# Kernel tuning notes

Measured on AMD Instinct MI355X. Metric: run time of the kernel, lower is better.

## Reference

```python
import jax, jax.numpy as jnp
import numpy as np

E = 1024   # embedding_dim
H = 16     # num_head
D = 64     # dim_head (E == H*D)
R = 8      # LoRA rank
BATCH = 2
SEQ = 2048
EPS = 1e-6


def setup_inputs() -> dict:
    key = jax.random.key(0)
    ks = jax.random.split(key, 16)
    s = 0.02
    return {
        "y": jax.random.normal(ks[0], (BATCH, SEQ, E), jnp.float32),
        "Wqkv": jax.random.normal(ks[1], (3 * E, E), jnp.float32) * s,
        "bqkv": jax.random.normal(ks[2], (3 * E,), jnp.float32) * s,
        "Wmsa": jax.random.normal(ks[3], (E, E), jnp.float32) * s,
        "Bq": jax.random.normal(ks[4], (E, R), jnp.float32) * s,
        "Aq": jax.random.normal(ks[5], (R, E), jnp.float32) * s,
        "Bk": jax.random.normal(ks[6], (E, R), jnp.float32) * s,
        "Ak": jax.random.normal(ks[7], (R, E), jnp.float32) * s,
        "Bv": jax.random.normal(ks[8], (E, R), jnp.float32) * s,
        "Av": jax.random.normal(ks[9], (R, E), jnp.float32) * s,
        "Bo": jax.random.normal(ks[10], (E, R), jnp.float32) * s,
        "Ao": jax.random.normal(ks[11], (R, E), jnp.float32) * s,
        "gamma": jnp.ones((E,), jnp.float32),
        "beta": jnp.zeros((E,), jnp.float32),
        "i": 0,
    }


def reference(y, Wqkv, bqkv, Wmsa, Bq, Aq, Bk, Ak, Bv, Av, Bo, Ao, gamma, beta, i):
    B, S, En = y.shape
    # fused QKV projection: nn.Linear -> y @ W.T + b
    qkv = (y @ Wqkv.T + bqkv).reshape(B, S, 3, H, D).transpose(2, 0, 3, 1, 4)
    Q, K, V = qkv[0], qkv[1], qkv[2]          # each [B,H,S,D]

    def lora_delta(Bw, Aw):
        # torch: y @ (B.weight @ A.weight), reshaped to heads
        return (y @ (Bw @ Aw)).reshape(B, S, H, D).transpose(0, 2, 1, 3)

    Q = Q + lora_delta(Bq, Aq)
    K = K + lora_delta(Bk, Ak)
    V = V + lora_delta(Bv, Av)

    scale = jnp.asarray(np.sqrt(D), y.dtype)
    scores = jnp.einsum('bhqd,bhkd->bhqk', Q, K) / scale
    attn = jax.nn.softmax(scores, axis=-1)
    o = jnp.einsum('bhqk,bhkd->bhqd', attn, V)          # [B,H,S,D]
    o = o.transpose(0, 2, 1, 3).reshape(B, S, H * D)    # [B,S,E]

    msa = o @ Wmsa.T + o @ (Bo @ Ao)
    res = msa + y

    mu = jnp.mean(res, axis=-1, keepdims=True)
    var = jnp.var(res, axis=-1, keepdims=True)
    return (res - mu) * jax.lax.rsqrt(var + EPS) * gamma + beta
```

## Files before the change

kernel.cpp:

```cpp
#include <hip/hip_runtime.h>
#include <hip/hip_bf16.h>
#include <stdint.h>

typedef __attribute__((ext_vector_type(8))) short short8;
typedef __attribute__((ext_vector_type(4))) float f32x4;

typedef const __attribute__((address_space(1))) void gv_t;
typedef __attribute__((address_space(3))) void lv_t;

#define SCQ 0.18033688011112042f

__device__ __forceinline__ void gl_lds16(const void* g, void* l) {
    __builtin_amdgcn_global_load_lds((gv_t*)g, (lv_t*)l, 16, 0, 0);
}

__device__ __forceinline__ unsigned short f2bf(float f) {
    union { float f; unsigned int u; } v; v.f = f;
    unsigned int r = v.u + 0x7fffu + ((v.u >> 16) & 1u);
    return (unsigned short)(r >> 16);
}

__device__ __forceinline__ unsigned int pack2bf(float a, float b) {
    union { __hip_bfloat162 h2; unsigned int u; } cv;
    cv.h2 = __float22bfloat162_rn(make_float2(a, b));
    return cv.u;
}

__device__ __forceinline__ f32x4 zero4() { f32x4 z = {0.f, 0.f, 0.f, 0.f}; return z; }

__global__ void k_prep(const float* __restrict__ y,
                       const float* __restrict__ Wqkv, const float* __restrict__ Wmsa,
                       const float* __restrict__ Bq, const float* __restrict__ Aq,
                       const float* __restrict__ Bk, const float* __restrict__ Ak,
                       const float* __restrict__ Bv, const float* __restrict__ Av,
                       const float* __restrict__ Bo, const float* __restrict__ Ao,
                       unsigned short* __restrict__ wout, unsigned short* __restrict__ yb) {
    const int bid = blockIdx.x;
    if (bid < 16384) {
        int idx = bid * 256 + threadIdx.x;
        int n = idx >> 10, k = idx & 1023;
        int sel = n >> 10, n0 = n & 1023;
        const float* Bp = (sel == 0) ? Bq : (sel == 1) ? Bk : (sel == 2) ? Bv : Bo;
        const float* Ap = (sel == 0) ? Aq : (sel == 1) ? Ak : (sel == 2) ? Av : Ao;
        float acc = (sel < 3) ? Wqkv[idx] : Wmsa[idx - 3145728];
        #pragma unroll
        for (int r = 0; r < 8; ++r) acc += Bp[k * 8 + r] * Ap[r * 1024 + n0];
        wout[idx] = f2bf(acc * ((sel == 0) ? SCQ : 1.0f));
    } else {
        int i = ((bid - 16384) * 256 + threadIdx.x) * 4;
        float4 v = *(const float4*)(y + i);
        union { unsigned short u[4]; uint2 w; } o;
        o.u[0] = f2bf(v.x); o.u[1] = f2bf(v.y); o.u[2] = f2bf(v.z); o.u[3] = f2bf(v.w);
        *(uint2*)(yb + i) = o.w;
    }
}

template <int TM, int EPI, int MINW>
__global__ __launch_bounds__(256, MINW) void k_gemm(const unsigned short* __restrict__ Ag,
                                                    const unsigned short* __restrict__ Bg,
                                                    const float* __restrict__ bias,
                                                    const float* __restrict__ yres,
                                                    unsigned short* __restrict__ vtg,
                                                    void* __restrict__ Cout,
                                                    int M, int N, int K) {
    constexpr int WAVES_N = 256 / TM;
    constexpr int WN = TM / 2;
    constexpr int NI = WN / 16;
    constexpr int ACALLS = TM / 64;
    __shared__ unsigned short As[2][TM * 32];
    __shared__ unsigned short Bs[2][128 * 32];
    const int flat = threadIdx.x;
    const int m0 = blockIdx.y * TM, n0 = blockIdx.x * 128;
    const int lane = flat & 63, wave = flat >> 6;
    const int l16 = lane & 15, quad = lane >> 4;
    const int wm = (wave / WAVES_N) * 64, wn = (wave % WAVES_N) * WN;

    f32x4 acc[4][NI];
    #pragma unroll
    for (int mi = 0; mi < 4; ++mi)
        #pragma unroll
        for (int ni = 0; ni < NI; ++ni) acc[mi][ni] = zero4();

    const unsigned short* ap = Ag + (size_t)(m0 + (flat >> 2)) * K + (flat & 3) * 8;
    const unsigned short* bp = Bg + (size_t)(n0 + (flat >> 2)) * K + (flat & 3) * 8;
    const size_t rstep = (size_t)64 * K;

    #pragma unroll
    for (int c = 0; c < ACALLS; ++c) gl_lds16(ap + c * rstep, &As[0][c * 2048 + flat * 8]);
    gl_lds16(bp,         &Bs[0][flat * 8]);
    gl_lds16(bp + rstep, &Bs[0][2048 + flat * 8]);
    ap += 32; bp += 32;
    __syncthreads();

    for (int k0 = 0; k0 < K; k0 += 32) {
        const int cur = (k0 >> 5) & 1;
        if (k0 + 32 < K) {
            const int nxt = cur ^ 1;
            #pragma unroll
            for (int c = 0; c < ACALLS; ++c) gl_lds16(ap + c * rstep, &As[nxt][c * 2048 + flat * 8]);
            gl_lds16(bp,         &Bs[nxt][flat * 8]);
            gl_lds16(bp + rstep, &Bs[nxt][2048 + flat * 8]);
            ap += 32; bp += 32;
        }

        short8 af[4], bfr[NI];
        #pragma unroll
        for (int i = 0; i < 4; ++i) af[i] = *(const short8*)&As[cur][(wm + i * 16 + l16) * 32 + quad * 8];
        #pragma unroll
        for (int i = 0; i < NI; ++i) bfr[i] = *(const short8*)&Bs[cur][(wn + i * 16 + l16) * 32 + quad * 8];
        #pragma unroll
        for (int mi = 0; mi < 4; ++mi)
            #pragma unroll
            for (int ni = 0; ni < NI; ++ni)
                acc[mi][ni] = __builtin_amdgcn_mfma_f32_16x16x32_bf16(af[mi], bfr[ni], acc[mi][ni], 0, 0, 0);

        __syncthreads();
    }

    if (EPI == 0) {
        unsigned short* C = (unsigned short*)Cout;
        if (n0 < 2048) {
            #pragma unroll
            for (int ni = 0; ni < NI; ++ni) {
                int col = n0 + wn + ni * 16 + l16;
                float bv = bias[col] * ((col < 1024) ? SCQ : 1.0f);
                #pragma unroll
                for (int mi = 0; mi < 4; ++mi) {
                    int row = m0 + wm + mi * 16 + quad * 4;
                    #pragma unroll
                    for (int r = 0; r < 4; ++r)
                        C[(size_t)(row + r) * N + col] = f2bf(acc[mi][ni][r] + bv);
                }
            }
        } else {
            #pragma unroll
            for (int ni = 0; ni < NI; ++ni) {
                int col = n0 + wn + ni * 16 + l16;
                float bv = bias[col];
                int hh = (col - 2048) >> 6, dd = col & 63;
                unsigned short* vrow0 = vtg + (size_t)(hh * 64 + dd) * 2048;
                #pragma unroll
                for (int mi = 0; mi < 4; ++mi) {
                    int row = m0 + wm + mi * 16 + quad * 4;
                    int bb = row >> 11, ss = row & 2047;
                    uint2 w;
                    w.x = pack2bf(acc[mi][ni][0] + bv, acc[mi][ni][1] + bv);
                    w.y = pack2bf(acc[mi][ni][2] + bv, acc[mi][ni][3] + bv);
                    *(uint2*)(vrow0 + (size_t)bb * 2097152 + ss) = w;
                }
            }
        }
    } else {
        float* C = (float*)Cout;
        #pragma unroll
        for (int ni = 0; ni < NI; ++ni) {
            int col = n0 + wn + ni * 16 + l16;
            #pragma unroll
            for (int mi = 0; mi < 4; ++mi) {
                int row = m0 + wm + mi * 16 + quad * 4;
                #pragma unroll
                for (int r = 0; r < 4; ++r)
                    C[(size_t)(row + r) * N + col] = acc[mi][ni][r] + yres[(size_t)(row + r) * N + col];
            }
        }
    }
}

__global__ __launch_bounds__(256, 3) void k_attn(const unsigned short* __restrict__ qkv,
                                                 const unsigned short* __restrict__ vtg,
                                                 unsigned short* __restrict__ o) {
    __shared__ unsigned short LDS[24576];
    unsigned short* Qs = LDS;
    unsigned short* Ps = LDS;
    unsigned short* Ks0 = LDS + 8192;
    unsigned short* Vt0 = LDS + 16384;

    const int t = threadIdx.x;
    const int lane = t & 63, wave = t >> 6;
    const int l16 = lane & 15, quad = lane >> 4;
    const int l8 = l16 & 7;
    const int q0 = blockIdx.x * 128;
    const int h = blockIdx.y, b = blockIdx.z;

    const unsigned short* qbase = qkv + (size_t)(b * 2048) * 3072 + h * 64;
    const unsigned short* kbase = qbase + 1024;
    const unsigned short* vtbase = vtg + (size_t)((b * 16 + h) * 64) * 2048;

    #pragma unroll
    for (int i = 0; i < 4; ++i) {
        int B = i * 256 + t;
        int row = B >> 3, c = (B & 7) ^ (row & 7);
        gl_lds16(qbase + (size_t)(q0 + row) * 3072 + c * 8, &Qs[B * 8]);
    }

    const int B0 = t, B1 = t + 256;
    const int r0 = B0 >> 3, c0 = (B0 & 7) ^ (r0 & 7);
    const int r1 = B1 >> 3, c1 = (B1 & 7) ^ (r1 & 7);
    const unsigned short* kp0 = kbase + (size_t)r0 * 3072 + c0 * 8;
    const unsigned short* kp1 = kbase + (size_t)r1 * 3072 + c1 * 8;
    const unsigned short* vp0 = vtbase + (size_t)r0 * 2048 + c0 * 8;
    const unsigned short* vp1 = vtbase + (size_t)r1 * 2048 + c1 * 8;

    gl_lds16(kp0, &Ks0[B0 * 8]);
    gl_lds16(kp1, &Ks0[B1 * 8]);
    gl_lds16(vp0, &Vt0[B0 * 8]);
    gl_lds16(vp1, &Vt0[B1 * 8]);
    kp0 += 64 * 3072; kp1 += 64 * 3072; vp0 += 64; vp1 += 64;

    __syncthreads();

    short8 qf[2][2];
    #pragma unroll
    for (int ni = 0; ni < 2; ++ni)
        #pragma unroll
        for (int kk = 0; kk < 2; ++kk)
            qf[ni][kk] = *(const short8*)&Qs[(wave * 32 + ni * 16 + l16) * 64 + ((kk * 4 + quad) ^ l8) * 8];

    __syncthreads();

    f32x4 acc_o[2][4];
    #pragma unroll
    for (int mo = 0; mo < 2; ++mo)
        #pragma unroll
        for (int nd = 0; nd < 4; ++nd) acc_o[mo][nd] = zero4();
    f32x4 acc_l[2] = {zero4(), zero4()};
    short8 ones;
    #pragma unroll
    for (int i = 0; i < 8; ++i) ones[i] = (short)0x3F80;

    for (int j = 0; j < 32; ++j) {
        const unsigned short* Ks = Ks0 + (j & 1) * 4096;
        const unsigned short* Vt = Vt0 + (j & 1) * 4096;

        if (j < 31) {
            unsigned short* Kn = Ks0 + ((j + 1) & 1) * 4096;
            unsigned short* Vn = Vt0 + ((j + 1) & 1) * 4096;
            gl_lds16(kp0, &Kn[B0 * 8]);
            gl_lds16(kp1, &Kn[B1 * 8]);
            gl_lds16(vp0, &Vn[B0 * 8]);
            gl_lds16(vp1, &Vn[B1 * 8]);
            kp0 += 64 * 3072; kp1 += 64 * 3072; vp0 += 64; vp1 += 64;
        }

        f32x4 sacc[4][2];
        #pragma unroll
        for (int mi = 0; mi < 4; ++mi)
            #pragma unroll
            for (int ni = 0; ni < 2; ++ni) sacc[mi][ni] = zero4();
        #pragma unroll
        for (int kk = 0; kk < 2; ++kk)
            #pragma unroll
            for (int mi = 0; mi < 4; ++mi) {
                short8 kf = *(const short8*)&Ks[(mi * 16 + l16) * 64 + ((kk * 4 + quad) ^ l8) * 8];
                #pragma unroll
                for (int ni = 0; ni < 2; ++ni)
                    sacc[mi][ni] = __builtin_amdgcn_mfma_f32_16x16x32_bf16(kf, qf[ni][kk], sacc[mi][ni], 0, 0, 0);
            }

        #pragma unroll
        for (int ni = 0; ni < 2; ++ni) {
            int qrow = wave * 32 + ni * 16 + l16;
            #pragma unroll
            for (int mi = 0; mi < 4; ++mi) {
                float p0 = __builtin_amdgcn_exp2f(sacc[mi][ni][0]);
                float p1 = __builtin_amdgcn_exp2f(sacc[mi][ni][1]);
                float p2 = __builtin_amdgcn_exp2f(sacc[mi][ni][2]);
                float p3 = __builtin_amdgcn_exp2f(sacc[mi][ni][3]);
                uint2 w; w.x = pack2bf(p0, p1); w.y = pack2bf(p2, p3);
                *(uint2*)&Ps[qrow * 64 + ((2 * mi + (quad >> 1)) ^ l8) * 8 + (quad & 1) * 4] = w;
            }
        }

        #pragma unroll
        for (int kk = 0; kk < 2; ++kk) {
            short8 pf[2];
            #pragma unroll
            for (int mo = 0; mo < 2; ++mo) {
                pf[mo] = *(const short8*)&Ps[(wave * 32 + mo * 16 + l16) * 64 + ((kk * 4 + quad) ^ l8) * 8];
                acc_l[mo] = __builtin_amdgcn_mfma_f32_16x16x32_bf16(pf[mo], ones, acc_l[mo], 0, 0, 0);
            }
            #pragma unroll
            for (int nd = 0; nd < 4; ++nd) {
                short8 vf = *(const short8*)&Vt[(nd * 16 + l16) * 64 + ((kk * 4 + quad) ^ l8) * 8];
                #pragma unroll
                for (int mo = 0; mo < 2; ++mo)
                    acc_o[mo][nd] = __builtin_amdgcn_mfma_f32_16x16x32_bf16(pf[mo], vf, acc_o[mo][nd], 0, 0, 0);
            }
        }

        __syncthreads();
    }

    #pragma unroll
    for (int mo = 0; mo < 2; ++mo)
        #pragma unroll
        for (int rr = 0; rr < 4; ++rr) {
            float inv = 1.0f / acc_l[mo][rr];
            int qg = q0 + wave * 32 + mo * 16 + quad * 4 + rr;
            size_t base = ((size_t)(b * 2048 + qg)) * 1024 + h * 64;
            #pragma unroll
            for (int nd = 0; nd < 4; ++nd)
                o[base + nd * 16 + l16] = f2bf(acc_o[mo][nd][rr] * inv);
        }
}

__global__ __launch_bounds__(256) void k_ln(const float* __restrict__ res,
                                            const float* __restrict__ g,
                                            const float* __restrict__ be,
                                            float* __restrict__ out) {
    __shared__ float red[8];
    const int row = blockIdx.x, t = threadIdx.x;
    const float* x = res + (size_t)row * 1024;
    float4 v = *(const float4*)(x + t * 4);
    float s = v.x + v.y + v.z + v.w;
    float sq = v.x * v.x + v.y * v.y + v.z * v.z + v.w * v.w;
    #pragma unroll
    for (int off = 32; off; off >>= 1) { s += __shfl_down(s, off); sq += __shfl_down(sq, off); }
    if ((t & 63) == 0) { red[t >> 6] = s; red[4 + (t >> 6)] = sq; }
    __syncthreads();
    float ts = red[0] + red[1] + red[2] + red[3];
    float tq = red[4] + red[5] + red[6] + red[7];
    float mu = ts * (1.f / 1024.f);
    float var = tq * (1.f / 1024.f) - mu * mu;
    float rstd = rsqrtf(var + 1e-6f);
    float4 gg = *(const float4*)(g + t * 4);
    float4 bb = *(const float4*)(be + t * 4);
    float4 ov;
    ov.x = (v.x - mu) * rstd * gg.x + bb.x;
    ov.y = (v.y - mu) * rstd * gg.y + bb.y;
    ov.z = (v.z - mu) * rstd * gg.z + bb.z;
    ov.w = (v.w - mu) * rstd * gg.w + bb.w;
    *(float4*)(out + (size_t)row * 1024 + t * 4) = ov;
}

extern "C" void kernel_launch(void* const* d_in, const int* in_sizes, int n_in,
                              void* d_out, int out_size, void* d_ws, size_t ws_size,
                              hipStream_t stream) {
    (void)in_sizes; (void)n_in; (void)out_size; (void)ws_size;
    const float* y    = (const float*)d_in[0];
    const float* Wqkv = (const float*)d_in[1];
    const float* bqkv = (const float*)d_in[2];
    const float* Wmsa = (const float*)d_in[3];
    const float* Bq = (const float*)d_in[4];
    const float* Aq = (const float*)d_in[5];
    const float* Bk = (const float*)d_in[6];
    const float* Ak = (const float*)d_in[7];
    const float* Bv = (const float*)d_in[8];
    const float* Av = (const float*)d_in[9];
    const float* Bo = (const float*)d_in[10];
    const float* Ao = (const float*)d_in[11];
    const float* gamma = (const float*)d_in[12];
    const float* beta  = (const float*)d_in[13];

    char* ws = (char*)d_ws;
    unsigned short* yb   = (unsigned short*)(ws);
    unsigned short* weq  = (unsigned short*)(ws + (8u  << 20));
    unsigned short* qkv  = (unsigned short*)(ws + (16u << 20));
    unsigned short* vtg  = (unsigned short*)(ws + (40u << 20));
    unsigned short* wem  = weq + 3145728;
    unsigned short* obuf = yb;
    float* res = (float*)qkv;

    k_prep<<<17408, 256, 0, stream>>>(y, Wqkv, Wmsa, Bq, Aq, Bk, Ak, Bv, Av, Bo, Ao, weq, yb);
    k_gemm<128, 0, 3><<<dim3(24, 32), 256, 0, stream>>>(yb, weq, bqkv, nullptr, vtg, (void*)qkv, 4096, 3072, 1024);
    k_attn<<<dim3(16, 16, 2), 256, 0, stream>>>(qkv, vtg, obuf);
    k_gemm<64, 1, 4><<<dim3(8, 64), 256, 0, stream>>>(obuf, wem, nullptr, y, nullptr, (void*)res, 4096, 1024, 1024);
    k_ln  <<<4096, 256, 0, stream>>>(res, gamma, beta, (float*)d_out);
}
```

Before: 214.3 us.

## Split attention over KV halves with fp32 partials and a combine kernel

Each attention block now processes only half of the key sequence, doubling the grid so more CUs are occupied. Unnormalized partial outputs and row sums are written in fp32 and a new combine kernel sums them, normalizes, and converts to bf16. This relies on the softmax having no running max, so partials add directly. It adds extra global memory traffic for the partials and an additional kernel launch.

```diff
diff --git a/kernel.cpp b/kernel.cpp
--- a/kernel.cpp
+++ b/kernel.cpp
@@ -168,7 +168,9 @@
 
 __global__ __launch_bounds__(256, 3) void k_attn(const unsigned short* __restrict__ qkv,
                                                  const unsigned short* __restrict__ vtg,
-                                                 unsigned short* __restrict__ o) {
+                                                 float* __restrict__ op0,
+                                                 float* __restrict__ op1,
+                                                 float* __restrict__ lp) {
     __shared__ unsigned short LDS[24576];
     unsigned short* Qs = LDS;
     unsigned short* Ps = LDS;
@@ -180,7 +182,9 @@
     const int l16 = lane & 15, quad = lane >> 4;
     const int l8 = l16 & 7;
     const int q0 = blockIdx.x * 128;
-    const int h = blockIdx.y, b = blockIdx.z;
+    const int h = blockIdx.y;
+    const int b = blockIdx.z >> 1, ks = blockIdx.z & 1;
+    const int j0 = ks * 16;
 
     const unsigned short* qbase = qkv + (size_t)(b * 2048) * 3072 + h * 64;
     const unsigned short* kbase = qbase + 1024;
@@ -196,10 +200,10 @@
     const int B0 = t, B1 = t + 256;
     const int r0 = B0 >> 3, c0 = (B0 & 7) ^ (r0 & 7);
     const int r1 = B1 >> 3, c1 = (B1 & 7) ^ (r1 & 7);
-    const unsigned short* kp0 = kbase + (size_t)r0 * 3072 + c0 * 8;
-    const unsigned short* kp1 = kbase + (size_t)r1 * 3072 + c1 * 8;
-    const unsigned short* vp0 = vtbase + (size_t)r0 * 2048 + c0 * 8;
-    const unsigned short* vp1 = vtbase + (size_t)r1 * 2048 + c1 * 8;
+    const unsigned short* kp0 = kbase + (size_t)(j0 * 64 + r0) * 3072 + c0 * 8;
+    const unsigned short* kp1 = kbase + (size_t)(j0 * 64 + r1) * 3072 + c1 * 8;
+    const unsigned short* vp0 = vtbase + (size_t)r0 * 2048 + j0 * 64 + c0 * 8;
+    const unsigned short* vp1 = vtbase + (size_t)r1 * 2048 + j0 * 64 + c1 * 8;
 
     gl_lds16(kp0, &Ks0[B0 * 8]);
     gl_lds16(kp1, &Ks0[B1 * 8]);
@@ -228,11 +232,11 @@
     #pragma unroll
     for (int i = 0; i < 8; ++i) ones[i] = (short)0x3F80;
 
-    for (int j = 0; j < 32; ++j) {
+    for (int j = 0; j < 16; ++j) {
         const unsigned short* Ks = Ks0 + (j & 1) * 4096;
         const unsigned short* Vt = Vt0 + (j & 1) * 4096;
 
-        if (j < 31) {
+        if (j < 15) {
             unsigned short* Kn = Ks0 + ((j + 1) & 1) * 4096;
             unsigned short* Vn = Vt0 + ((j + 1) & 1) * 4096;
             gl_lds16(kp0, &Kn[B0 * 8]);
@@ -291,17 +295,37 @@
         __syncthreads();
     }
 
+    float* op = ks ? op1 : op0;
+    const size_t hb = ((size_t)(b * 16 + h)) * 2048;
     #pragma unroll
     for (int mo = 0; mo < 2; ++mo)
         #pragma unroll
         for (int rr = 0; rr < 4; ++rr) {
-            float inv = 1.0f / acc_l[mo][rr];
             int qg = q0 + wave * 32 + mo * 16 + quad * 4 + rr;
-            size_t base = ((size_t)(b * 2048 + qg)) * 1024 + h * 64;
+            float* row = op + (hb + qg) * 64;
             #pragma unroll
             for (int nd = 0; nd < 4; ++nd)
-                o[base + nd * 16 + l16] = f2bf(acc_o[mo][nd][rr] * inv);
-        }
+                row[nd * 16 + l16] = acc_o[mo][nd][rr];
+            if (l16 == 0)
+                lp[(size_t)ks * 65536 + hb + qg] = acc_l[mo][rr];
+        }
+}
+
+__global__ __launch_bounds__(256) void k_comb(const float* __restrict__ op0,
+                                              const float* __restrict__ op1,
+                                              const float* __restrict__ lp,
+                                              unsigned short* __restrict__ o) {
+    const int tok = blockIdx.x, t = threadIdx.x;
+    const int b = tok >> 11, s = tok & 2047, h = t >> 4;
+    const size_t hb = ((size_t)(b * 16 + h)) * 2048 + s;
+    const size_t base = hb * 64 + (t & 15) * 4;
+    float4 O0 = *(const float4*)(op0 + base);
+    float4 O1 = *(const float4*)(op1 + base);
+    float inv = 1.0f / (lp[hb] + lp[65536 + hb]);
+    uint2 w;
+    w.x = pack2bf((O0.x + O1.x) * inv, (O0.y + O1.y) * inv);
+    w.y = pack2bf((O0.z + O1.z) * inv, (O0.w + O1.w) * inv);
+    *(uint2*)(o + (size_t)tok * 1024 + t * 4) = w;
 }
 
 __global__ __launch_bounds__(256) void k_ln(const float* __restrict__ res,
@@ -357,13 +381,17 @@
     unsigned short* weq  = (unsigned short*)(ws + (8u  << 20));
     unsigned short* qkv  = (unsigned short*)(ws + (16u << 20));
     unsigned short* vtg  = (unsigned short*)(ws + (40u << 20));
+    float* op1 = (float*)(ws + (48u << 20));
+    float* lp  = (float*)(ws + (64u << 20));
     unsigned short* wem  = weq + 3145728;
     unsigned short* obuf = yb;
     float* res = (float*)qkv;
+    float* op0 = (float*)d_out;
 
     k_prep<<<17408, 256, 0, stream>>>(y, Wqkv, Wmsa, Bq, Aq, Bk, Ak, Bv, Av, Bo, Ao, weq, yb);
     k_gemm<128, 0, 3><<<dim3(24, 32), 256, 0, stream>>>(yb, weq, bqkv, nullptr, vtg, (void*)qkv, 4096, 3072, 1024);
-    k_attn<<<dim3(16, 16, 2), 256, 0, stream>>>(qkv, vtg, obuf);
+    k_attn<<<dim3(16, 16, 4), 256, 0, stream>>>(qkv, vtg, op0, op1, lp);
+    k_comb<<<4096, 256, 0, stream>>>(op0, op1, lp, obuf);
     k_gemm<64, 1, 4><<<dim3(8, 64), 256, 0, stream>>>(obuf, wem, nullptr, y, nullptr, (void*)res, 4096, 1024, 1024);
     k_ln  <<<4096, 256, 0, stream>>>(res, gamma, beta, (float*)d_out);
 }
```

Measured after the change: 220.5 us. 2.9% more time.

## Software-pipeline attention PV with double-buffered P and vectorize weight prep

Applied to the files above, without the earlier changes.

The attention loop now computes QK^T for block j while running the P·V MFMAs for block j-1. P gets two buffers and V^T gets three rotating buffers, which removes one barrier per iteration and lets exp/softmax work overlap with matrix ops. The extra buffers raise LDS use to 72KB per block, and launch bounds drop from 3 to 2 blocks per CU, so occupancy may fall. The prep kernel also handles four weights per thread with float4 loads and packed bf16 stores, cutting its grid size.

```diff
diff --git a/kernel.cpp b/kernel.cpp
--- a/kernel.cpp
+++ b/kernel.cpp
@@ -36,22 +36,31 @@
                        const float* __restrict__ Bo, const float* __restrict__ Ao,
                        unsigned short* __restrict__ wout, unsigned short* __restrict__ yb) {
     const int bid = blockIdx.x;
-    if (bid < 16384) {
-        int idx = bid * 256 + threadIdx.x;
-        int n = idx >> 10, k = idx & 1023;
+    if (bid < 4096) {
+        int base = (bid * 256 + threadIdx.x) * 4;
+        int n = base >> 10, k = base & 1023;
         int sel = n >> 10, n0 = n & 1023;
         const float* Bp = (sel == 0) ? Bq : (sel == 1) ? Bk : (sel == 2) ? Bv : Bo;
         const float* Ap = (sel == 0) ? Aq : (sel == 1) ? Ak : (sel == 2) ? Av : Ao;
-        float acc = (sel < 3) ? Wqkv[idx] : Wmsa[idx - 3145728];
-        #pragma unroll
-        for (int r = 0; r < 8; ++r) acc += Bp[k * 8 + r] * Ap[r * 1024 + n0];
-        wout[idx] = f2bf(acc * ((sel == 0) ? SCQ : 1.0f));
+        float4 w = (sel < 3) ? *(const float4*)(Wqkv + base)
+                             : *(const float4*)(Wmsa + base - 3145728);
+        float a0 = w.x, a1 = w.y, a2 = w.z, a3 = w.w;
+        #pragma unroll
+        for (int r = 0; r < 8; ++r) {
+            float ap = Ap[r * 1024 + n0];
+            a0 += Bp[(k + 0) * 8 + r] * ap;
+            a1 += Bp[(k + 1) * 8 + r] * ap;
+            a2 += Bp[(k + 2) * 8 + r] * ap;
+            a3 += Bp[(k + 3) * 8 + r] * ap;
+        }
+        float sc = (sel == 0) ? SCQ : 1.0f;
+        uint2 ww; ww.x = pack2bf(a0 * sc, a1 * sc); ww.y = pack2bf(a2 * sc, a3 * sc);
+        *(uint2*)(wout + base) = ww;
     } else {
-        int i = ((bid - 16384) * 256 + threadIdx.x) * 4;
+        int i = ((bid - 4096) * 256 + threadIdx.x) * 4;
         float4 v = *(const float4*)(y + i);
-        union { unsigned short u[4]; uint2 w; } o;
-        o.u[0] = f2bf(v.x); o.u[1] = f2bf(v.y); o.u[2] = f2bf(v.z); o.u[3] = f2bf(v.w);
-        *(uint2*)(yb + i) = o.w;
+        uint2 ww; ww.x = pack2bf(v.x, v.y); ww.y = pack2bf(v.z, v.w);
+        *(uint2*)(yb + i) = ww;
     }
 }
 
@@ -166,14 +175,14 @@
     }
 }
 
-__global__ __launch_bounds__(256, 3) void k_attn(const unsigned short* __restrict__ qkv,
+__global__ __launch_bounds__(256, 2) void k_attn(const unsigned short* __restrict__ qkv,
                                                  const unsigned short* __restrict__ vtg,
                                                  unsigned short* __restrict__ o) {
-    __shared__ unsigned short LDS[24576];
-    unsigned short* Qs = LDS;
-    unsigned short* Ps = LDS;
-    unsigned short* Ks0 = LDS + 8192;
-    unsigned short* Vt0 = LDS + 16384;
+    __shared__ unsigned short LDS[36864];
+    unsigned short* Qs  = LDS;
+    unsigned short* PsB = LDS;
+    unsigned short* KsB = LDS + 16384;
+    unsigned short* VtB = LDS + 24576;
 
     const int t = threadIdx.x;
     const int lane = t & 63, wave = t >> 6;
@@ -201,10 +210,10 @@
     const unsigned short* vp0 = vtbase + (size_t)r0 * 2048 + c0 * 8;
     const unsigned short* vp1 = vtbase + (size_t)r1 * 2048 + c1 * 8;
 
-    gl_lds16(kp0, &Ks0[B0 * 8]);
-    gl_lds16(kp1, &Ks0[B1 * 8]);
-    gl_lds16(vp0, &Vt0[B0 * 8]);
-    gl_lds16(vp1, &Vt0[B1 * 8]);
+    gl_lds16(kp0, &KsB[B0 * 8]);
+    gl_lds16(kp1, &KsB[B1 * 8]);
+    gl_lds16(vp0, &VtB[B0 * 8]);
+    gl_lds16(vp1, &VtB[B1 * 8]);
     kp0 += 64 * 3072; kp1 += 64 * 3072; vp0 += 64; vp1 += 64;
 
     __syncthreads();
@@ -215,8 +224,6 @@
         #pragma unroll
         for (int kk = 0; kk < 2; ++kk)
             qf[ni][kk] = *(const short8*)&Qs[(wave * 32 + ni * 16 + l16) * 64 + ((kk * 4 + quad) ^ l8) * 8];
-
-    __syncthreads();
 
     f32x4 acc_o[2][4];
     #pragma unroll
@@ -229,12 +236,9 @@
     for (int i = 0; i < 8; ++i) ones[i] = (short)0x3F80;
 
     for (int j = 0; j < 32; ++j) {
-        const unsigned short* Ks = Ks0 + (j & 1) * 4096;
-        const unsigned short* Vt = Vt0 + (j & 1) * 4096;
-
         if (j < 31) {
-            unsigned short* Kn = Ks0 + ((j + 1) & 1) * 4096;
-            unsigned short* Vn = Vt0 + ((j + 1) & 1) * 4096;
+            unsigned short* Kn = KsB + ((j + 1) & 1) * 4096;
+            unsigned short* Vn = VtB + ((j + 1) % 3) * 4096;
             gl_lds16(kp0, &Kn[B0 * 8]);
             gl_lds16(kp1, &Kn[B1 * 8]);
             gl_lds16(vp0, &Vn[B0 * 8]);
@@ -242,6 +246,7 @@
             kp0 += 64 * 3072; kp1 += 64 * 3072; vp0 += 64; vp1 += 64;
         }
 
+        const unsigned short* Ks = KsB + (j & 1) * 4096;
         f32x4 sacc[4][2];
         #pragma unroll
         for (int mi = 0; mi < 4; ++mi)
@@ -257,6 +262,28 @@
                     sacc[mi][ni] = __builtin_amdgcn_mfma_f32_16x16x32_bf16(kf, qf[ni][kk], sacc[mi][ni], 0, 0, 0);
             }
 
+        if (j > 0) {
+            const unsigned short* Pp = PsB + ((j - 1) & 1) * 8192;
+            const unsigned short* Vt = VtB + ((j - 1) % 3) * 4096;
+            #pragma unroll
+            for (int kk = 0; kk < 2; ++kk) {
+                short8 pf[2];
+                #pragma unroll
+                for (int mo = 0; mo < 2; ++mo) {
+                    pf[mo] = *(const short8*)&Pp[(wave * 32 + mo * 16 + l16) * 64 + ((kk * 4 + quad) ^ l8) * 8];
+                    acc_l[mo] = __builtin_amdgcn_mfma_f32_16x16x32_bf16(pf[mo], ones, acc_l[mo], 0, 0, 0);
+                }
+                #pragma unroll
+                for (int nd = 0; nd < 4; ++nd) {
+                    short8 vf = *(const short8*)&Vt[(nd * 16 + l16) * 64 + ((kk * 4 + quad) ^ l8) * 8];
+                    #pragma unroll
+                    for (int mo = 0; mo < 2; ++mo)
+                        acc_o[mo][nd] = __builtin_amdgcn_mfma_f32_16x16x32_bf16(pf[mo], vf, acc_o[mo][nd], 0, 0, 0);
+                }
+            }
+        }
+
+        unsigned short* Pw = PsB + (j & 1) * 8192;
         #pragma unroll
         for (int ni = 0; ni < 2; ++ni) {
             int qrow = wave * 32 + ni * 16 + l16;
@@ -267,16 +294,22 @@
                 float p2 = __builtin_amdgcn_exp2f(sacc[mi][ni][2]);
                 float p3 = __builtin_amdgcn_exp2f(sacc[mi][ni][3]);
                 uint2 w; w.x = pack2bf(p0, p1); w.y = pack2bf(p2, p3);
-                *(uint2*)&Ps[qrow * 64 + ((2 * mi + (quad >> 1)) ^ l8) * 8 + (quad & 1) * 4] = w;
-            }
-        }
-
+                *(uint2*)&Pw[qrow * 64 + ((2 * mi + (quad >> 1)) ^ l8) * 8 + (quad & 1) * 4] = w;
+            }
+        }
+
+        __syncthreads();
+    }
+
+    {
+        const unsigned short* Pp = PsB + 8192;
+        const unsigned short* Vt = VtB + 4096;
         #pragma unroll
         for (int kk = 0; kk < 2; ++kk) {
             short8 pf[2];
             #pragma unroll
             for (int mo = 0; mo < 2; ++mo) {
-                pf[mo] = *(const short8*)&Ps[(wave * 32 + mo * 16 + l16) * 64 + ((kk * 4 + quad) ^ l8) * 8];
+                pf[mo] = *(const short8*)&Pp[(wave * 32 + mo * 16 + l16) * 64 + ((kk * 4 + quad) ^ l8) * 8];
                 acc_l[mo] = __builtin_amdgcn_mfma_f32_16x16x32_bf16(pf[mo], ones, acc_l[mo], 0, 0, 0);
             }
             #pragma unroll
@@ -287,8 +320,6 @@
                     acc_o[mo][nd] = __builtin_amdgcn_mfma_f32_16x16x32_bf16(pf[mo], vf, acc_o[mo][nd], 0, 0, 0);
             }
         }
-
-        __syncthreads();
     }
 
     #pragma unroll
@@ -361,7 +392,7 @@
     unsigned short* obuf = yb;
     float* res = (float*)qkv;
 
-    k_prep<<<17408, 256, 0, stream>>>(y, Wqkv, Wmsa, Bq, Aq, Bk, Ak, Bv, Av, Bo, Ao, weq, yb);
+    k_prep<<<8192, 256, 0, stream>>>(y, Wqkv, Wmsa, Bq, Aq, Bk, Ak, Bv, Av, Bo, Ao, weq, yb);
     k_gemm<128, 0, 3><<<dim3(24, 32), 256, 0, stream>>>(yb, weq, bqkv, nullptr, vtg, (void*)qkv, 4096, 3072, 1024);
     k_attn<<<dim3(16, 16, 2), 256, 0, stream>>>(qkv, vtg, obuf);
     k_gemm<64, 1, 4><<<dim3(8, 64), 256, 0, stream>>>(obuf, wem, nullptr, y, nullptr, (void*)res, 4096, 1024, 1024);
```

Measured after the change: 222.9 us. 1.04x slower.
